# Kernel tuning notes

Hardware: AMD Instinct MI355X
Metric: run time of the kernel (lower is better)

## Reference

```python
import jax, jax.numpy as jnp
import numpy as np


def setup_inputs() -> dict:
    key = jax.random.key(0)
    k1, _ = jax.random.split(key)
    B, S, D = 4, 4096, 64
    inp = jax.random.normal(k1, (B, S, D), dtype=jnp.float32)
    attn_mask = jnp.zeros((S, S), dtype=bool)  # no masked positions
    return {"input": inp, "attn_mask": attn_mask}


def reference(input, attn_mask):
    # attn_mask: bool [S,S] -> additive mask with -inf at masked positions
    am = jnp.where(attn_mask, -jnp.inf, 0.0).T  # transpose(0,1)
    # scores: [B,S,S]
    v = jnp.einsum('bsd,btd->bst', input, input)
    mask = (1.0 - am) * -10000.0
    v = v + mask  # dead in original module too: w is drawn fresh below
    # w = empty_like(v).uniform_(-0.1, 0.1)
    wkey = jax.random.key(42)
    w = jax.random.uniform(wkey, v.shape, dtype=v.dtype, minval=-0.1, maxval=0.1)
    w = jax.nn.softmax(w, axis=-1)
    # per-column (dim 1) L1 renorm: w[:, i] /= ||w[:, i]||_1 over (batch, last dim)
    denom = jnp.sum(jnp.abs(w), axis=(0, 2), keepdims=True)  # [1,S,1]
    w = w / denom
    return jnp.einsum('bst,btd->bsd', w, input)
```

## Files before the change

### kernel.cpp

```cpp
#include <hip/hip_runtime.h>
#include <hip/hip_bf16.h>
#include <stdint.h>


#define S_ 4096
#define D_ 64

#define EXP_A ((float)(0.2 * 1.4426950408889634 / 8388608.0))
#define EXP_B ((float)(-0.1 * 1.4426950408889634))

typedef __attribute__((ext_vector_type(8))) short short8v;
typedef __attribute__((ext_vector_type(4))) float floatx4;

__device__ __forceinline__ void tf2(uint32_t f0, uint32_t f1,
                                    uint32_t& r0, uint32_t& r1) {
    const uint32_t k1 = 42u, k2 = 0x1BD11BDAu ^ 42u;
    uint32_t a0 = 0u,      b0 = f0 + k1;
    uint32_t a1 = 0u,      b1 = f1 + k1;
#define R2(r) { a0 += b0; a1 += b1;                         \
                b0 = __builtin_rotateleft32(b0, (r));       \
                b1 = __builtin_rotateleft32(b1, (r));       \
                b0 ^= a0; b1 ^= a1; }
    R2(13) R2(15) R2(26) R2(6)
    a0 += k1; b0 += k2 + 1u;   a1 += k1; b1 += k2 + 1u;
    R2(17) R2(29) R2(16) R2(24)
    a0 += k2; b0 += 2u;        a1 += k2; b1 += 2u;
    R2(13) R2(15) R2(26) R2(6)
    b0 += k1 + 3u;             b1 += k1 + 3u;
    R2(17) R2(29) R2(16) R2(24)
    a0 += k1; b0 += k2 + 4u;   a1 += k1; b1 += k2 + 4u;
    R2(13) R2(15) R2(26) R2(6)
    a0 += k2; b0 += 5u;        a1 += k2; b1 += 5u;
#undef R2
    r0 = a0 ^ b0;
    r1 = a1 ^ b1;
}

__device__ __forceinline__ float uexp(uint32_t bits) {
    const float fm = (float)(bits >> 9);
    const float arg = __builtin_fmaf(fm, EXP_A, EXP_B);
    return __builtin_amdgcn_exp2f(arg);
}

__device__ __forceinline__ uint32_t cvt_pk_bf16(float e0, float e1) {
    uint32_t r;
    asm("v_cvt_pk_bf16_f32 %0, %1, %2" : "=v"(r) : "v"(e0), "v"(e1));
    return r;
}

__device__ __forceinline__ short8v gen_a(uint32_t c0, float& zp0, float& zp1) {
    union { uint32_t u[4]; short8v v; } a;
#pragma unroll
    for (int jp = 0; jp < 4; ++jp) {
        uint32_t r0, r1;
        tf2(c0 + 2u * jp, c0 + 2u * jp + 1u, r0, r1);
        const float e0 = uexp(r0);
        const float e1 = uexp(r1);
        zp0 += e0;
        zp1 += e1;
        a.u[jp] = cvt_pk_bf16(e0, e1);
    }
    return a.v;
}

__global__ __launch_bounds__(64) void pack_xt_bf16(
    const float* __restrict__ x, short* __restrict__ bf)
{
    const int id = blockIdx.x;
    const int l  = threadIdx.x;
    const int dg = id & 3;
    const int kc = (id >> 2) & 1;
    const int kt = (id >> 3) & 63;
    const int b  = id >> 9;
    const int d  = dg * 16 + (l & 15);
    const int k0 = kt * 64 + kc * 32 + (l >> 4) * 8;
    const float* __restrict__ xb = x + (size_t)b * (S_ * D_);
    union { short8v v; short s[8]; } r;
#pragma unroll
    for (int j = 0; j < 8; ++j) {
        __hip_bfloat16 h = __float2bfloat16(xb[(size_t)(k0 + j) * D_ + d]);
        r.s[j] = __builtin_bit_cast(short, h);
    }
    *(short8v*)&bf[(size_t)id * 512 + l * 8] = r.v;
}

__global__ __launch_bounds__(512, 8) void fused_rand_attn_mfma4(
    const short* __restrict__ bf, float* __restrict__ out)
{
    const int tid  = threadIdx.x;
    const int bid  = (blockIdx.x & 7) * 128 + (blockIdx.x >> 3);
    const int b    = bid >> 8;
    const int s0   = (bid & 255) * 16;
    const int w    = tid >> 6;
    const int lane = tid & 63;
    const int lt   = lane & 15;
    const int lh   = lane >> 4;

    __shared__ float ACC[8][4][64][4];
    __shared__ float ZL[8][16];

    floatx4 acc0 = {0.f,0.f,0.f,0.f}, acc1 = {0.f,0.f,0.f,0.f};
    floatx4 acc2 = {0.f,0.f,0.f,0.f}, acc3 = {0.f,0.f,0.f,0.f};
    float zpA = 0.f, zpB = 0.f;

    const short* __restrict__ bl =
        bf + (size_t)b * (64 * 4096) + (size_t)lane * 8;
    const uint32_t fl = (((uint32_t)b << 24) | ((uint32_t)(s0 + lt) << 12))
                        + (uint32_t)(lh * 8);

#pragma unroll 1
    for (int kt = w; kt < 64; kt += 8) {
        const short* pk = bl + (size_t)kt * 4096;
        const uint32_t kb = fl + ((uint32_t)kt << 6);

        const short8v b00 = *(const short8v*)(pk);
        const short8v b10 = *(const short8v*)(pk + 512);
        const short8v b20 = *(const short8v*)(pk + 1024);
        const short8v b30 = *(const short8v*)(pk + 1536);

        const short8v a0 = gen_a(kb, zpA, zpB);

        const short8v b01 = *(const short8v*)(pk + 2048);
        const short8v b11 = *(const short8v*)(pk + 2560);
        const short8v b21 = *(const short8v*)(pk + 3072);
        const short8v b31 = *(const short8v*)(pk + 3584);

        acc0 = __builtin_amdgcn_mfma_f32_16x16x32_bf16(a0, b00, acc0, 0, 0, 0);
        acc1 = __builtin_amdgcn_mfma_f32_16x16x32_bf16(a0, b10, acc1, 0, 0, 0);
        acc2 = __builtin_amdgcn_mfma_f32_16x16x32_bf16(a0, b20, acc2, 0, 0, 0);
        acc3 = __builtin_amdgcn_mfma_f32_16x16x32_bf16(a0, b30, acc3, 0, 0, 0);

        const short8v a1 = gen_a(kb + 32u, zpA, zpB);

        acc0 = __builtin_amdgcn_mfma_f32_16x16x32_bf16(a1, b01, acc0, 0, 0, 0);
        acc1 = __builtin_amdgcn_mfma_f32_16x16x32_bf16(a1, b11, acc1, 0, 0, 0);
        acc2 = __builtin_amdgcn_mfma_f32_16x16x32_bf16(a1, b21, acc2, 0, 0, 0);
        acc3 = __builtin_amdgcn_mfma_f32_16x16x32_bf16(a1, b31, acc3, 0, 0, 0);
    }

    float zp = zpA + zpB;
    zp += __shfl_xor(zp, 16);
    zp += __shfl_xor(zp, 32);
    if (lane < 16) ZL[w][lane] = zp;
    *(floatx4*)&ACC[w][0][lane][0] = acc0;
    *(floatx4*)&ACC[w][1][lane][0] = acc1;
    *(floatx4*)&ACC[w][2][lane][0] = acc2;
    *(floatx4*)&ACC[w][3][lane][0] = acc3;
    __syncthreads();

    const int dg = w & 3;
    const int rh = w >> 2;
    floatx4 facc = {0.f,0.f,0.f,0.f};
#pragma unroll
    for (int w2 = 0; w2 < 8; ++w2) {
        const floatx4 t = *(const floatx4*)&ACC[w2][dg][lane][0];
        facc.x += t.x; facc.y += t.y; facc.z += t.z; facc.w += t.w;
    }
    const float v0 = rh ? facc.z : facc.x;
    const float v1 = rh ? facc.w : facc.y;
    const int row0 = lh * 4 + rh * 2;
    float Z0 = 0.f, Z1 = 0.f;
#pragma unroll
    for (int w2 = 0; w2 < 8; ++w2) {
        Z0 += ZL[w2][row0];
        Z1 += ZL[w2][row0 + 1];
    }
    const int col = dg * 16 + lt;
    out[((size_t)b * S_ + (s0 + row0)) * D_ + col]     = v0 * (0.25f / Z0);
    out[((size_t)b * S_ + (s0 + row0 + 1)) * D_ + col] = v1 * (0.25f / Z1);
}

extern "C" void kernel_launch(void* const* d_in, const int* in_sizes, int n_in,
                              void* d_out, int out_size, void* d_ws, size_t ws_size,
                              hipStream_t stream) {
    const float* x = (const float*)d_in[0];
    float* out = (float*)d_out;
    short* bfw = (short*)d_ws;
    (void)in_sizes; (void)n_in; (void)out_size; (void)ws_size;
    hipLaunchKernelGGL(pack_xt_bf16, dim3(2048), dim3(64), 0, stream, x, bfw);
    hipLaunchKernelGGL(fused_rand_attn_mfma4, dim3(1024), dim3(512), 0, stream,
                       bfw, out);
}
```

Baseline: 135.8 us.

## Compute softmax row sums via MFMA with ones and widen Threefry batching

Replaces the per-lane scalar accumulation of softmax denominators with an extra MFMA against a bf16 ones vector. The denominator now sums the bf16-rounded weights, which keeps it consistent with the numerator. Threefry is restructured to generate 8 counters in one interleaved batch for more ILP. The uniform-to-float path drops the shift and scales the full 32-bit value instead. Occupancy hint is lowered from 8 to 4 waves per EU to allow more registers, at the cost of fewer resident waves to hide latency.

```diff
diff --git a/kernel.cpp b/kernel.cpp
--- a/kernel.cpp
+++ b/kernel.cpp
@@ -6,40 +6,41 @@
 #define S_ 4096
 #define D_ 64
 
-#define EXP_A ((float)(0.2 * 1.4426950408889634 / 8388608.0))
-#define EXP_B ((float)(-0.1 * 1.4426950408889634))
+#define EXP_A32 ((float)(0.2 * 1.4426950408889634 / 4294967296.0))
+#define EXP_B   ((float)(-0.1 * 1.4426950408889634))
 
 typedef __attribute__((ext_vector_type(8))) short short8v;
 typedef __attribute__((ext_vector_type(4))) float floatx4;
 
-__device__ __forceinline__ void tf2(uint32_t f0, uint32_t f1,
-                                    uint32_t& r0, uint32_t& r1) {
+__device__ __forceinline__ void tf8(uint32_t c0, uint32_t r[8]) {
     const uint32_t k1 = 42u, k2 = 0x1BD11BDAu ^ 42u;
-    uint32_t a0 = 0u,      b0 = f0 + k1;
-    uint32_t a1 = 0u,      b1 = f1 + k1;
-#define R2(r) { a0 += b0; a1 += b1;                         \
-                b0 = __builtin_rotateleft32(b0, (r));       \
-                b1 = __builtin_rotateleft32(b1, (r));       \
-                b0 ^= a0; b1 ^= a1; }
-    R2(13) R2(15) R2(26) R2(6)
-    a0 += k1; b0 += k2 + 1u;   a1 += k1; b1 += k2 + 1u;
-    R2(17) R2(29) R2(16) R2(24)
-    a0 += k2; b0 += 2u;        a1 += k2; b1 += 2u;
-    R2(13) R2(15) R2(26) R2(6)
-    b0 += k1 + 3u;             b1 += k1 + 3u;
-    R2(17) R2(29) R2(16) R2(24)
-    a0 += k1; b0 += k2 + 4u;   a1 += k1; b1 += k2 + 4u;
-    R2(13) R2(15) R2(26) R2(6)
-    a0 += k2; b0 += 5u;        a1 += k2; b1 += 5u;
-#undef R2
-    r0 = a0 ^ b0;
-    r1 = a1 ^ b1;
-}
-
-__device__ __forceinline__ float uexp(uint32_t bits) {
-    const float fm = (float)(bits >> 9);
-    const float arg = __builtin_fmaf(fm, EXP_A, EXP_B);
-    return __builtin_amdgcn_exp2f(arg);
+    uint32_t a[8], b[8];
+#pragma unroll
+    for (int i = 0; i < 8; ++i) { a[i] = 0u; b[i] = c0 + (uint32_t)i + k1; }
+#define TF_RND(rot)                                          \
+    _Pragma("unroll")                                        \
+    for (int i = 0; i < 8; ++i) {                            \
+        a[i] += b[i];                                        \
+        b[i] = __builtin_rotateleft32(b[i], (rot));          \
+        b[i] ^= a[i];                                        \
+    }
+#define TF_INJ(ka, kb)                                       \
+    _Pragma("unroll")                                        \
+    for (int i = 0; i < 8; ++i) { a[i] += (ka); b[i] += (kb); }
+    TF_RND(13) TF_RND(15) TF_RND(26) TF_RND(6)
+    TF_INJ(k1, k2 + 1u)
+    TF_RND(17) TF_RND(29) TF_RND(16) TF_RND(24)
+    TF_INJ(k2, 2u)
+    TF_RND(13) TF_RND(15) TF_RND(26) TF_RND(6)
+    TF_INJ(0u, k1 + 3u)
+    TF_RND(17) TF_RND(29) TF_RND(16) TF_RND(24)
+    TF_INJ(k1, k2 + 4u)
+    TF_RND(13) TF_RND(15) TF_RND(26) TF_RND(6)
+    TF_INJ(k2, 5u)
+#undef TF_RND
+#undef TF_INJ
+#pragma unroll
+    for (int i = 0; i < 8; ++i) r[i] = a[i] ^ b[i];
 }
 
 __device__ __forceinline__ uint32_t cvt_pk_bf16(float e0, float e1) {
@@ -48,18 +49,18 @@
     return r;
 }
 
-__device__ __forceinline__ short8v gen_a(uint32_t c0, float& zp0, float& zp1) {
+__device__ __forceinline__ short8v gen_a(uint32_t c0) {
+    uint32_t r[8];
+    tf8(c0, r);
+    float e[8];
+#pragma unroll
+    for (int i = 0; i < 8; ++i) {
+        const float fm = (float)r[i];
+        e[i] = __builtin_amdgcn_exp2f(__builtin_fmaf(fm, EXP_A32, EXP_B));
+    }
     union { uint32_t u[4]; short8v v; } a;
 #pragma unroll
-    for (int jp = 0; jp < 4; ++jp) {
-        uint32_t r0, r1;
-        tf2(c0 + 2u * jp, c0 + 2u * jp + 1u, r0, r1);
-        const float e0 = uexp(r0);
-        const float e1 = uexp(r1);
-        zp0 += e0;
-        zp1 += e1;
-        a.u[jp] = cvt_pk_bf16(e0, e1);
-    }
+    for (int i = 0; i < 4; ++i) a.u[i] = cvt_pk_bf16(e[2 * i], e[2 * i + 1]);
     return a.v;
 }
 
@@ -84,7 +85,7 @@
     *(short8v*)&bf[(size_t)id * 512 + l * 8] = r.v;
 }
 
-__global__ __launch_bounds__(512, 8) void fused_rand_attn_mfma4(
+__global__ __launch_bounds__(512, 4) void fused_rand_attn_mfma5(
     const short* __restrict__ bf, float* __restrict__ out)
 {
     const int tid  = threadIdx.x;
@@ -101,7 +102,11 @@
 
     floatx4 acc0 = {0.f,0.f,0.f,0.f}, acc1 = {0.f,0.f,0.f,0.f};
     floatx4 acc2 = {0.f,0.f,0.f,0.f}, acc3 = {0.f,0.f,0.f,0.f};
-    float zpA = 0.f, zpB = 0.f;
+    floatx4 accz = {0.f,0.f,0.f,0.f};
+
+    const short one_bf = (short)0x3F80;
+    const short8v bones = {one_bf, one_bf, one_bf, one_bf,
+                           one_bf, one_bf, one_bf, one_bf};
 
     const short* __restrict__ bl =
         bf + (size_t)b * (64 * 4096) + (size_t)lane * 8;
@@ -117,31 +122,30 @@
         const short8v b10 = *(const short8v*)(pk + 512);
         const short8v b20 = *(const short8v*)(pk + 1024);
         const short8v b30 = *(const short8v*)(pk + 1536);
-
-        const short8v a0 = gen_a(kb, zpA, zpB);
-
         const short8v b01 = *(const short8v*)(pk + 2048);
         const short8v b11 = *(const short8v*)(pk + 2560);
         const short8v b21 = *(const short8v*)(pk + 3072);
         const short8v b31 = *(const short8v*)(pk + 3584);
 
+        const short8v a0 = gen_a(kb);
+        const short8v a1 = gen_a(kb + 32u);
+
         acc0 = __builtin_amdgcn_mfma_f32_16x16x32_bf16(a0, b00, acc0, 0, 0, 0);
         acc1 = __builtin_amdgcn_mfma_f32_16x16x32_bf16(a0, b10, acc1, 0, 0, 0);
         acc2 = __builtin_amdgcn_mfma_f32_16x16x32_bf16(a0, b20, acc2, 0, 0, 0);
         acc3 = __builtin_amdgcn_mfma_f32_16x16x32_bf16(a0, b30, acc3, 0, 0, 0);
-
-        const short8v a1 = gen_a(kb + 32u, zpA, zpB);
-
+        accz = __builtin_amdgcn_mfma_f32_16x16x32_bf16(a0, bones, accz, 0, 0, 0);
         acc0 = __builtin_amdgcn_mfma_f32_16x16x32_bf16(a1, b01, acc0, 0, 0, 0);
         acc1 = __builtin_amdgcn_mfma_f32_16x16x32_bf16(a1, b11, acc1, 0, 0, 0);
         acc2 = __builtin_amdgcn_mfma_f32_16x16x32_bf16(a1, b21, acc2, 0, 0, 0);
         acc3 = __builtin_amdgcn_mfma_f32_16x16x32_bf16(a1, b31, acc3, 0, 0, 0);
+        accz = __builtin_amdgcn_mfma_f32_16x16x32_bf16(a1, bones, accz, 0, 0, 0);
     }
 
-    float zp = zpA + zpB;
-    zp += __shfl_xor(zp, 16);
-    zp += __shfl_xor(zp, 32);
-    if (lane < 16) ZL[w][lane] = zp;
+    if (lt == 0) {
+#pragma unroll
+        for (int r = 0; r < 4; ++r) ZL[w][lh * 4 + r] = accz[r];
+    }
     *(floatx4*)&ACC[w][0][lane][0] = acc0;
     *(floatx4*)&ACC[w][1][lane][0] = acc1;
     *(floatx4*)&ACC[w][2][lane][0] = acc2;
@@ -178,6 +182,6 @@
     short* bfw = (short*)d_ws;
     (void)in_sizes; (void)n_in; (void)out_size; (void)ws_size;
     hipLaunchKernelGGL(pack_xt_bf16, dim3(2048), dim3(64), 0, stream, x, bfw);
-    hipLaunchKernelGGL(fused_rand_attn_mfma4, dim3(1024), dim3(512), 0, stream,
+    hipLaunchKernelGGL(fused_rand_attn_mfma5, dim3(1024), dim3(512), 0, stream,
                        bfw, out);
 }
```

Result: no change. 133.9 us, median of 3 (-1.4%).
